# Performance work log

Hardware: AMD Instinct MI355X
Metric: run time of the kernel (lower is better)

The kernel has to match this reference:

```python
import jax, jax.numpy as jnp
import numpy as np

FACTOR = 5  # routing softmax power


def setup_inputs() -> dict:
    key = jax.random.key(0)
    kq, kk, kv = jax.random.split(key, 3)
    B, L, S, H, E, D = 2, 2048, 2048, 16, 64, 64
    queries = jax.random.normal(kq, (B, L, H, E), dtype=jnp.float32)
    keys = jax.random.normal(kk, (B, S, H, E), dtype=jnp.float32)
    values = jax.random.normal(kv, (B, S, H, D), dtype=jnp.float32)
    return {"queries": queries, "keys": keys, "values": values}


def reference(queries, keys, values):
    # NOTE: original computes scale = 1/sqrt(E) but never applies it; faithful.
    # Original computes the same unscaled QK^T twice; compute once and reuse.
    scores = jnp.einsum('blhe,bshe->bhls', queries, keys)  # [B,H,L,S]
    dense = jax.nn.softmax(scores, axis=-1)
    routing = dense ** FACTOR  # softmax(scores)**factor == routing_scores
    combined = (routing + dense) * 0.5
    sparse = combined / jnp.sum(combined, axis=-1, keepdims=True)
    V = jnp.einsum('bhls,bshd->blhd', sparse, values)  # [B,L,H,D]
    return V
```

## Files before the change

### kernel.cpp

```cpp
#include <hip/hip_runtime.h>
#include <math.h>


typedef _Float16 h8 __attribute__((ext_vector_type(8)));
typedef _Float16 h4 __attribute__((ext_vector_type(4)));
typedef _Float16 h2 __attribute__((ext_vector_type(2)));
typedef float f4 __attribute__((ext_vector_type(4)));

constexpr int Bc = 2, Lc = 2048, Sc = 2048, Hc = 16, Ec = 64, Dc = 64;
constexpr int QB = 128, KB = 64, NT = Sc / KB;
constexpr float LOG2E = 1.4426950408889634f;

__device__ __forceinline__ f4 mm(h8 a, h8 b, f4 c) {
  return __builtin_amdgcn_mfma_f32_16x16x32_f16(a, b, c, 0, 0, 0);
}

__global__ __launch_bounds__(256, 2) void dsa_mfma(
    const float* __restrict__ Q, const float* __restrict__ K,
    const float* __restrict__ V, float* __restrict__ O) {
  __shared__ __align__(16) _Float16 Ks[64 * 64];
  __shared__ __align__(16) _Float16 Vts[64 * 64];
  __shared__ __align__(16) _Float16 Ps[4][2][32 * 64];

  const int tid = threadIdx.x;
  const int w = tid >> 6, lane = tid & 63, lq = lane & 15, lg = lane >> 4;
  const int kxor = (lq & 7) << 3;

  const int blk = blockIdx.x;
  const int ww = (blk & 7) * 64 + (blk >> 3);
  const int qtb = ww & 15, bh = ww >> 4;
  const int b = bh >> 4, h = bh & 15;

  const size_t qbase = (size_t)b * Lc * Hc * Ec + (size_t)h * Ec;
  const size_t kbase = (size_t)b * Sc * Hc * Ec + (size_t)h * Ec;
  const size_t vbase = (size_t)b * Sc * Hc * Dc + (size_t)h * Dc;
  const int q0 = qtb * QB + w * 32;

  h8 qf[2][2];
#pragma unroll
  for (int qt = 0; qt < 2; ++qt)
#pragma unroll
    for (int ks = 0; ks < 2; ++ks) {
      const float* p = Q + qbase + (size_t)(q0 + qt * 16 + lq) * 1024 + ks * 32 + lg * 8;
      f4 a = *(const f4*)p, c = *(const f4*)(p + 4);
#pragma unroll
      for (int i = 0; i < 4; ++i) {
        qf[qt][ks][i] = (_Float16)(a[i] * LOG2E);
        qf[qt][ks][4 + i] = (_Float16)(c[i] * LOG2E);
      }
    }

  f4 O1[4][2] = {}, O5[4][2] = {};
  float mr[2] = {-INFINITY, -INFINITY}, S1[2] = {0.f, 0.f}, S5[2] = {0.f, 0.f};

  f4 kf[4], va[2], vb[2];

  auto LOADK = [&](int k0) {
#pragma unroll
    for (int i = 0; i < 4; ++i) {
      int idx = i * 256 + tid;
      int krow = idx >> 4, kc4 = idx & 15;
      kf[i] = *(const f4*)(K + kbase + (size_t)(k0 + krow) * 1024 + kc4 * 4);
    }
  };
  auto LOADV = [&](int k0) {
#pragma unroll
    for (int i = 0; i < 2; ++i) {
      int idx = i * 256 + tid;
      int dq = idx & 15, kp = idx >> 4;
      const float* p = V + vbase + (size_t)(k0 + 2 * kp) * 1024 + dq * 4;
      va[i] = *(const f4*)p;
      vb[i] = *(const f4*)(p + 1024);
    }
  };
  auto STORE = [&]() {
#pragma unroll
    for (int i = 0; i < 4; ++i) {
      int idx = i * 256 + tid;
      int krow = idx >> 4, kc4 = idx & 15;
      int col = (kc4 * 4) ^ ((krow & 7) << 3);
      h4 hh;
#pragma unroll
      for (int j = 0; j < 4; ++j) hh[j] = (_Float16)kf[i][j];
      *(h4*)&Ks[krow * 64 + col] = hh;
    }
#pragma unroll
    for (int i = 0; i < 2; ++i) {
      int idx = i * 256 + tid;
      int dq = idx & 15, kp = idx >> 4;
#pragma unroll
      for (int j = 0; j < 4; ++j) {
        int d = dq * 4 + j;
        int col = (2 * kp) ^ ((d & 7) << 3);
        h2 hh = {(_Float16)va[i][j], (_Float16)vb[i][j]};
        *(h2*)&Vts[d * 64 + col] = hh;
      }
    }
  };

  LOADK(0);
  LOADV(0);

#pragma unroll 1
  for (int ks = 0; ks < NT; ++ks) {
    __syncthreads();
    STORE();
    if (ks + 1 < NT) {
      LOADK((ks + 1) * KB);
      LOADV((ks + 1) * KB);
    }
    __syncthreads();

    f4 sc[2][4] = {};
#pragma unroll
    for (int kk = 0; kk < 2; ++kk)
#pragma unroll
      for (int mt = 0; mt < 4; ++mt) {
        h8 kf8 = *(const h8*)&Ks[(mt * 16 + lq) * 64 + ((kk * 32 + lg * 8) ^ kxor)];
        sc[0][mt] = mm(kf8, qf[0][kk], sc[0][mt]);
        sc[1][mt] = mm(kf8, qf[1][kk], sc[1][mt]);
      }

#pragma unroll
    for (int qt = 0; qt < 2; ++qt) {
      float tm = -INFINITY;
#pragma unroll
      for (int mt = 0; mt < 4; ++mt)
#pragma unroll
        for (int r = 0; r < 4; ++r) tm = fmaxf(tm, sc[qt][mt][r]);
      tm = fmaxf(tm, __shfl_xor(tm, 16));
      tm = fmaxf(tm, __shfl_xor(tm, 32));
      if (__any(tm > mr[qt])) {
        float nm = fmaxf(mr[qt], tm);
        float f = __builtin_amdgcn_exp2f(mr[qt] - nm);
        float f2 = f * f, f5 = f2 * f2 * f;
        mr[qt] = nm;
        S1[qt] *= f;
        S5[qt] *= f5;
#pragma unroll
        for (int dt = 0; dt < 4; ++dt) {
          O1[dt][qt] *= f;
          O5[dt][qt] *= f5;
        }
      }
      float t1 = 0.f, t5 = 0.f;
#pragma unroll
      for (int mt = 0; mt < 4; ++mt) {
        h4 pe, p5;
#pragma unroll
        for (int r = 0; r < 4; ++r) {
          float e = __builtin_amdgcn_exp2f(sc[qt][mt][r] - mr[qt]);
          float e2 = e * e, e5v = e2 * e2 * e;
          t1 += e;
          t5 += e5v;
          pe[r] = (_Float16)e;
          p5[r] = (_Float16)e5v;
        }
        int pcol = (mt * 16 + lg * 4) ^ kxor;
        *(h4*)&Ps[w][0][(qt * 16 + lq) * 64 + pcol] = pe;
        *(h4*)&Ps[w][1][(qt * 16 + lq) * 64 + pcol] = p5;
      }
      t1 += __shfl_xor(t1, 16);
      t1 += __shfl_xor(t1, 32);
      t5 += __shfl_xor(t5, 16);
      t5 += __shfl_xor(t5, 32);
      S1[qt] += t1;
      S5[qt] += t5;
    }

#pragma unroll
    for (int k2 = 0; k2 < 2; ++k2) {
      h8 vf[4];
#pragma unroll
      for (int dt = 0; dt < 4; ++dt)
        vf[dt] = *(const h8*)&Vts[(dt * 16 + lq) * 64 + ((k2 * 32 + lg * 8) ^ kxor)];
#pragma unroll
      for (int qt = 0; qt < 2; ++qt) {
        h8 be = *(const h8*)&Ps[w][0][(qt * 16 + lq) * 64 + ((k2 * 32 + lg * 8) ^ kxor)];
        h8 b5 = *(const h8*)&Ps[w][1][(qt * 16 + lq) * 64 + ((k2 * 32 + lg * 8) ^ kxor)];
#pragma unroll
        for (int dt = 0; dt < 4; ++dt) {
          O1[dt][qt] = mm(vf[dt], be, O1[dt][qt]);
          O5[dt][qt] = mm(vf[dt], b5, O5[dt][qt]);
        }
      }
    }
  }

  const size_t obase = (size_t)b * Lc * Hc * Dc + (size_t)h * Dc;
#pragma unroll
  for (int qt = 0; qt < 2; ++qt) {
    float z = S1[qt], z2 = z * z, z4 = z2 * z2;
    float inv = 1.0f / (S5[qt] + z4 * S1[qt]);
#pragma unroll
    for (int dt = 0; dt < 4; ++dt) {
      f4 o = (O5[dt][qt] + z4 * O1[dt][qt]) * inv;
      *(f4*)(O + obase + (size_t)(q0 + qt * 16 + lq) * 1024 + dt * 16 + lg * 4) = o;
    }
  }
}

extern "C" void kernel_launch(void* const* d_in, const int* in_sizes, int n_in,
                              void* d_out, int out_size, void* d_ws, size_t ws_size,
                              hipStream_t stream) {
  const float* q = (const float*)d_in[0];
  const float* k = (const float*)d_in[1];
  const float* v = (const float*)d_in[2];
  float* o = (float*)d_out;
  dsa_mfma<<<dim3(512), dim3(256), 0, stream>>>(q, k, v, o);
}
```

Before: 95.90 us.

## Halve per-wave query rows, double blocks, pack conversions, add MFMA priority

Each wave now handles 16 query rows instead of 32, so a block covers 64 queries and the grid doubles to 1024 blocks. Launch bounds rise to 4 blocks per CU and the P buffer shrinks accordingly, aiming for more occupancy and latency hiding. V is loaded column-wise so each thread writes a full h8 into the transposed tile, fp16 conversions use packed cvt_pkrtz, and s_setprio is raised around the MFMA loops. The trade-off is that each K/V tile is loaded and converted twice as often per query, roughly doubling global/LDS staging traffic, and cvt_pkrtz rounds toward zero.

Measured after the change: 103.1 us. 7.5% more time.

```diff
diff --git a/kernel.cpp b/kernel.cpp
--- a/kernel.cpp
+++ b/kernel.cpp
@@ -7,94 +7,91 @@
 typedef _Float16 h2 __attribute__((ext_vector_type(2)));
 typedef float f4 __attribute__((ext_vector_type(4)));
 
-constexpr int Bc = 2, Lc = 2048, Sc = 2048, Hc = 16, Ec = 64, Dc = 64;
-constexpr int QB = 128, KB = 64, NT = Sc / KB;
+constexpr int Lc = 2048, Sc = 2048, Hc = 16;
+constexpr int KB = 64, NT = Sc / KB;
 constexpr float LOG2E = 1.4426950408889634f;
 
 __device__ __forceinline__ f4 mm(h8 a, h8 b, f4 c) {
   return __builtin_amdgcn_mfma_f32_16x16x32_f16(a, b, c, 0, 0, 0);
 }
-
-__global__ __launch_bounds__(256, 2) void dsa_mfma(
+__device__ __forceinline__ h2 pk(float a, float b) {
+  return __builtin_bit_cast(h2, __builtin_amdgcn_cvt_pkrtz(a, b));
+}
+
+__global__ __launch_bounds__(256, 4) void dsa_mfma(
     const float* __restrict__ Q, const float* __restrict__ K,
     const float* __restrict__ V, float* __restrict__ O) {
   __shared__ __align__(16) _Float16 Ks[64 * 64];
   __shared__ __align__(16) _Float16 Vts[64 * 64];
-  __shared__ __align__(16) _Float16 Ps[4][2][32 * 64];
+  __shared__ __align__(16) _Float16 Ps[4][2][16 * 64];
 
   const int tid = threadIdx.x;
   const int w = tid >> 6, lane = tid & 63, lq = lane & 15, lg = lane >> 4;
   const int kxor = (lq & 7) << 3;
 
   const int blk = blockIdx.x;
-  const int ww = (blk & 7) * 64 + (blk >> 3);
-  const int qtb = ww & 15, bh = ww >> 4;
+  const int ww = (blk & 7) * 128 + (blk >> 3);
+  const int qtb = ww & 31, bh = ww >> 5;
   const int b = bh >> 4, h = bh & 15;
 
-  const size_t qbase = (size_t)b * Lc * Hc * Ec + (size_t)h * Ec;
-  const size_t kbase = (size_t)b * Sc * Hc * Ec + (size_t)h * Ec;
-  const size_t vbase = (size_t)b * Sc * Hc * Dc + (size_t)h * Dc;
-  const int q0 = qtb * QB + w * 32;
-
-  h8 qf[2][2];
-#pragma unroll
-  for (int qt = 0; qt < 2; ++qt)
-#pragma unroll
-    for (int ks = 0; ks < 2; ++ks) {
-      const float* p = Q + qbase + (size_t)(q0 + qt * 16 + lq) * 1024 + ks * 32 + lg * 8;
-      f4 a = *(const f4*)p, c = *(const f4*)(p + 4);
-#pragma unroll
-      for (int i = 0; i < 4; ++i) {
-        qf[qt][ks][i] = (_Float16)(a[i] * LOG2E);
-        qf[qt][ks][4 + i] = (_Float16)(c[i] * LOG2E);
-      }
-    }
-
-  f4 O1[4][2] = {}, O5[4][2] = {};
-  float mr[2] = {-INFINITY, -INFINITY}, S1[2] = {0.f, 0.f}, S5[2] = {0.f, 0.f};
-
-  f4 kf[4], va[2], vb[2];
+  const size_t base = ((size_t)b * Sc * Hc + h) * 64;
+  const float* Qb = Q + base;
+  const float* Kb = K + base;
+  const float* Vb = V + base;
+  const int q0 = qtb * 64 + w * 16;
+
+  h8 qf[2];
+#pragma unroll
+  for (int kk = 0; kk < 2; ++kk) {
+    const float* p = Qb + (size_t)(q0 + lq) * 1024 + kk * 32 + lg * 8;
+    f4 a = *(const f4*)p, c = *(const f4*)(p + 4);
+#pragma unroll
+    for (int i = 0; i < 4; ++i) {
+      qf[kk][i] = (_Float16)(a[i] * LOG2E);
+      qf[kk][4 + i] = (_Float16)(c[i] * LOG2E);
+    }
+  }
+
+  f4 O1[4] = {}, O5[4] = {};
+  float mr = -INFINITY, S1 = 0.f, S5 = 0.f;
+
+  f4 kf[4];
+  float vreg[2][8];
+  const int krow_ = tid >> 4, kc4 = tid & 15;
+  const int vd = tid & 63, vo0 = (tid >> 6) * 2;
 
   auto LOADK = [&](int k0) {
 #pragma unroll
-    for (int i = 0; i < 4; ++i) {
-      int idx = i * 256 + tid;
-      int krow = idx >> 4, kc4 = idx & 15;
-      kf[i] = *(const f4*)(K + kbase + (size_t)(k0 + krow) * 1024 + kc4 * 4);
-    }
+    for (int i = 0; i < 4; ++i)
+      kf[i] = *(const f4*)(Kb + (size_t)(k0 + i * 16 + krow_) * 1024 + kc4 * 4);
   };
   auto LOADV = [&](int k0) {
 #pragma unroll
     for (int i = 0; i < 2; ++i) {
-      int idx = i * 256 + tid;
-      int dq = idx & 15, kp = idx >> 4;
-      const float* p = V + vbase + (size_t)(k0 + 2 * kp) * 1024 + dq * 4;
-      va[i] = *(const f4*)p;
-      vb[i] = *(const f4*)(p + 1024);
+      const float* p = Vb + (size_t)(k0 + (vo0 + i) * 8) * 1024 + vd;
+#pragma unroll
+      for (int j = 0; j < 8; ++j) vreg[i][j] = p[(size_t)j * 1024];
     }
   };
   auto STORE = [&]() {
 #pragma unroll
     for (int i = 0; i < 4; ++i) {
-      int idx = i * 256 + tid;
-      int krow = idx >> 4, kc4 = idx & 15;
-      int col = (kc4 * 4) ^ ((krow & 7) << 3);
-      h4 hh;
-#pragma unroll
-      for (int j = 0; j < 4; ++j) hh[j] = (_Float16)kf[i][j];
-      *(h4*)&Ks[krow * 64 + col] = hh;
+      int krow = i * 16 + krow_;
+      h2 a = pk(kf[i][0], kf[i][1]);
+      h2 bb = pk(kf[i][2], kf[i][3]);
+      h4 hh = {a[0], a[1], bb[0], bb[1]};
+      *(h4*)&Ks[krow * 64 + ((kc4 * 4) ^ ((krow & 7) << 3))] = hh;
     }
 #pragma unroll
     for (int i = 0; i < 2; ++i) {
-      int idx = i * 256 + tid;
-      int dq = idx & 15, kp = idx >> 4;
-#pragma unroll
-      for (int j = 0; j < 4; ++j) {
-        int d = dq * 4 + j;
-        int col = (2 * kp) ^ ((d & 7) << 3);
-        h2 hh = {(_Float16)va[i][j], (_Float16)vb[i][j]};
-        *(h2*)&Vts[d * 64 + col] = hh;
-      }
+      h8 hh;
+#pragma unroll
+      for (int u = 0; u < 4; ++u) {
+        h2 t = pk(vreg[i][2 * u], vreg[i][2 * u + 1]);
+        hh[2 * u] = t[0];
+        hh[2 * u + 1] = t[1];
+      }
+      *(h8*)&Vts[vd * 64 + (((vo0 + i) * 8) ^ ((vd & 7) << 3))] = hh;
     }
   };
 
@@ -111,92 +108,91 @@
     }
     __syncthreads();
 
-    f4 sc[2][4] = {};
+    f4 sc[4] = {};
+    __builtin_amdgcn_s_setprio(1);
 #pragma unroll
     for (int kk = 0; kk < 2; ++kk)
 #pragma unroll
       for (int mt = 0; mt < 4; ++mt) {
         h8 kf8 = *(const h8*)&Ks[(mt * 16 + lq) * 64 + ((kk * 32 + lg * 8) ^ kxor)];
-        sc[0][mt] = mm(kf8, qf[0][kk], sc[0][mt]);
-        sc[1][mt] = mm(kf8, qf[1][kk], sc[1][mt]);
-      }
-
-#pragma unroll
-    for (int qt = 0; qt < 2; ++qt) {
-      float tm = -INFINITY;
-#pragma unroll
-      for (int mt = 0; mt < 4; ++mt)
-#pragma unroll
-        for (int r = 0; r < 4; ++r) tm = fmaxf(tm, sc[qt][mt][r]);
-      tm = fmaxf(tm, __shfl_xor(tm, 16));
-      tm = fmaxf(tm, __shfl_xor(tm, 32));
-      if (__any(tm > mr[qt])) {
-        float nm = fmaxf(mr[qt], tm);
-        float f = __builtin_amdgcn_exp2f(mr[qt] - nm);
-        float f2 = f * f, f5 = f2 * f2 * f;
-        mr[qt] = nm;
-        S1[qt] *= f;
-        S5[qt] *= f5;
-#pragma unroll
-        for (int dt = 0; dt < 4; ++dt) {
-          O1[dt][qt] *= f;
-          O5[dt][qt] *= f5;
-        }
-      }
-      float t1 = 0.f, t5 = 0.f;
-#pragma unroll
-      for (int mt = 0; mt < 4; ++mt) {
-        h4 pe, p5;
-#pragma unroll
-        for (int r = 0; r < 4; ++r) {
-          float e = __builtin_amdgcn_exp2f(sc[qt][mt][r] - mr[qt]);
-          float e2 = e * e, e5v = e2 * e2 * e;
-          t1 += e;
-          t5 += e5v;
-          pe[r] = (_Float16)e;
-          p5[r] = (_Float16)e5v;
-        }
-        int pcol = (mt * 16 + lg * 4) ^ kxor;
-        *(h4*)&Ps[w][0][(qt * 16 + lq) * 64 + pcol] = pe;
-        *(h4*)&Ps[w][1][(qt * 16 + lq) * 64 + pcol] = p5;
-      }
-      t1 += __shfl_xor(t1, 16);
-      t1 += __shfl_xor(t1, 32);
-      t5 += __shfl_xor(t5, 16);
-      t5 += __shfl_xor(t5, 32);
-      S1[qt] += t1;
-      S5[qt] += t5;
-    }
+        sc[mt] = mm(kf8, qf[kk], sc[mt]);
+      }
+    __builtin_amdgcn_s_setprio(0);
+
+    float tm = -INFINITY;
+#pragma unroll
+    for (int mt = 0; mt < 4; ++mt)
+#pragma unroll
+      for (int r = 0; r < 4; ++r) tm = fmaxf(tm, sc[mt][r]);
+    tm = fmaxf(tm, __shfl_xor(tm, 16));
+    tm = fmaxf(tm, __shfl_xor(tm, 32));
+    if (__any(tm > mr)) {
+      float nm = fmaxf(mr, tm);
+      float f = __builtin_amdgcn_exp2f(mr - nm);
+      float f2 = f * f, f5 = f2 * f2 * f;
+      mr = nm;
+      S1 *= f;
+      S5 *= f5;
+#pragma unroll
+      for (int dt = 0; dt < 4; ++dt) {
+        O1[dt] *= f;
+        O5[dt] *= f5;
+      }
+    }
+    float t1 = 0.f, t5 = 0.f;
+#pragma unroll
+    for (int mt = 0; mt < 4; ++mt) {
+      float e[4], e5[4];
+#pragma unroll
+      for (int r = 0; r < 4; ++r) {
+        e[r] = __builtin_amdgcn_exp2f(sc[mt][r] - mr);
+        float e2 = e[r] * e[r];
+        e5[r] = e2 * e2 * e[r];
+        t1 += e[r];
+        t5 += e5[r];
+      }
+      h2 a = pk(e[0], e[1]);
+      h2 bb = pk(e[2], e[3]);
+      h4 pe = {a[0], a[1], bb[0], bb[1]};
+      h2 c = pk(e5[0], e5[1]);
+      h2 d = pk(e5[2], e5[3]);
+      h4 p5 = {c[0], c[1], d[0], d[1]};
+      int pcol = (mt * 16 + lg * 4) ^ kxor;
+      *(h4*)&Ps[w][0][lq * 64 + pcol] = pe;
+      *(h4*)&Ps[w][1][lq * 64 + pcol] = p5;
+    }
+    t1 += __shfl_xor(t1, 16);
+    t1 += __shfl_xor(t1, 32);
+    t5 += __shfl_xor(t5, 16);
+    t5 += __shfl_xor(t5, 32);
+    S1 += t1;
+    S5 += t5;
 
 #pragma unroll
     for (int k2 = 0; k2 < 2; ++k2) {
+      const int rc = (k2 * 32 + lg * 8) ^ kxor;
+      h8 be = *(const h8*)&Ps[w][0][lq * 64 + rc];
+      h8 b5 = *(const h8*)&Ps[w][1][lq * 64 + rc];
       h8 vf[4];
 #pragma unroll
       for (int dt = 0; dt < 4; ++dt)
-        vf[dt] = *(const h8*)&Vts[(dt * 16 + lq) * 64 + ((k2 * 32 + lg * 8) ^ kxor)];
-#pragma unroll
-      for (int qt = 0; qt < 2; ++qt) {
-        h8 be = *(const h8*)&Ps[w][0][(qt * 16 + lq) * 64 + ((k2 * 32 + lg * 8) ^ kxor)];
-        h8 b5 = *(const h8*)&Ps[w][1][(qt * 16 + lq) * 64 + ((k2 * 32 + lg * 8) ^ kxor)];
-#pragma unroll
-        for (int dt = 0; dt < 4; ++dt) {
-          O1[dt][qt] = mm(vf[dt], be, O1[dt][qt]);
-          O5[dt][qt] = mm(vf[dt], b5, O5[dt][qt]);
-        }
-      }
+        vf[dt] = *(const h8*)&Vts[(dt * 16 + lq) * 64 + rc];
+      __builtin_amdgcn_s_setprio(1);
+#pragma unroll
+      for (int dt = 0; dt < 4; ++dt) {
+        O1[dt] = mm(vf[dt], be, O1[dt]);
+        O5[dt] = mm(vf[dt], b5, O5[dt]);
+      }
+      __builtin_amdgcn_s_setprio(0);
     }
   }
 
-  const size_t obase = (size_t)b * Lc * Hc * Dc + (size_t)h * Dc;
-#pragma unroll
-  for (int qt = 0; qt < 2; ++qt) {
-    float z = S1[qt], z2 = z * z, z4 = z2 * z2;
-    float inv = 1.0f / (S5[qt] + z4 * S1[qt]);
-#pragma unroll
-    for (int dt = 0; dt < 4; ++dt) {
-      f4 o = (O5[dt][qt] + z4 * O1[dt][qt]) * inv;
-      *(f4*)(O + obase + (size_t)(q0 + qt * 16 + lq) * 1024 + dt * 16 + lg * 4) = o;
-    }
+  const float z = S1, z2 = z * z, z4 = z2 * z2;
+  const float inv = 1.0f / (S5 + z4 * S1);
+#pragma unroll
+  for (int dt = 0; dt < 4; ++dt) {
+    f4 o = (O5[dt] + z4 * O1[dt]) * inv;
+    *(f4*)(O + base + (size_t)(q0 + lq) * 1024 + dt * 16 + lg * 4) = o;
   }
 }
 
@@ -207,5 +203,5 @@
   const float* k = (const float*)d_in[1];
   const float* v = (const float*)d_in[2];
   float* o = (float*)d_out;
-  dsa_mfma<<<dim3(512), dim3(256), 0, stream>>>(q, k, v, o);
-}
+  dsa_mfma<<<dim3(1024), dim3(256), 0, stream>>>(q, k, v, o);
+}
```
